# Performance work log

Measured on AMD Instinct MI355X. Metric: run time of the kernel, lower is better.

The kernel has to match this reference:

```python
import jax, jax.numpy as jnp
import numpy as np

N = 100000      # nodes
E = 800000      # edges (nnz of sparse adj)
D_IN = 128      # input feature dim
H = 64          # hidden_units
EMB = 32        # embsize
N_IDX = 50000   # gathered output rows
EPS = 1e-05     # BatchNormalization epsilon


def spmm(rows, cols, vals, x):
    # out[i] = sum_{e: rows[e]==i} vals[e] * x[cols[e]]  == sparse A @ x
    return jax.ops.segment_sum(vals[:, None] * x[cols], rows, num_segments=N)


def batchnorm(x, gamma, beta):
    # training-mode BN over node (batch) axis, matching Keras BatchNormalization
    m = jnp.mean(x, axis=0)
    v = jnp.var(x, axis=0)
    return (x - m) * jax.lax.rsqrt(v + EPS) * gamma + beta


def setup_inputs() -> dict:
    key = jax.random.key(0)
    ks = jax.random.split(key, 16)
    def w(k, fan_in, shape):
        return jax.random.normal(k, shape, dtype=jnp.float32) / np.sqrt(fan_in)
    inp = {
        "features": jax.random.normal(ks[0], (N, D_IN), dtype=jnp.float32),
        "rows": jax.random.randint(ks[1], (E,), 0, N),
        "cols": jax.random.randint(ks[2], (E,), 0, N),
        "vals": jax.random.uniform(ks[3], (E,), dtype=jnp.float32),
        "idx": jax.random.randint(ks[4], (N_IDX,), 0, N),
        # layer 0 (Dense with bias since l==0)
        "Wn0": w(ks[5], D_IN, (D_IN, H)), "bn0": jnp.zeros((H,), jnp.float32),
        "Wg0": w(ks[6], D_IN, (D_IN, H)), "bg0": jnp.zeros((H,), jnp.float32),
        "ab0": jnp.zeros((H,), jnp.float32),  # BiasLayer after SpMM
        "g0": jnp.ones((H,), jnp.float32), "b0": jnp.zeros((H,), jnp.float32),
        # layer 1 (no Dense bias)
        "Wn1": w(ks[7], H, (H, H)),
        "Wg1": w(ks[8], H, (H, H)),
        "ab1": jnp.zeros((H,), jnp.float32),
        "g1": jnp.ones((H,), jnp.float32), "b1": jnp.zeros((H,), jnp.float32),
        # conv_last block (Dense use_bias=False)
        "WnL": w(ks[9], H, (H, EMB)),
        "WgL": w(ks[10], H, (H, EMB)),
        "abL": jnp.zeros((EMB,), jnp.float32),
    }
    return inp


def reference(features, rows, cols, vals, idx,
              Wn0, bn0, Wg0, bg0, ab0, g0, b0,
              Wn1, Wg1, ab1, g1, b1,
              WnL, WgL, abL):
    x = features
    # SAGE layer 0
    x_node = x @ Wn0 + bn0
    x_neigh = x @ Wg0 + bg0
    agg = spmm(rows, cols, vals, x_neigh) + ab0
    x = jax.nn.relu(batchnorm(x_node + agg, g0, b0))
    # SAGE layer 1
    x_node = x @ Wn1
    x_neigh = x @ Wg1
    agg = spmm(rows, cols, vals, x_neigh) + ab1
    x = jax.nn.relu(batchnorm(x_node + agg, g1, b1))
    # conv_last projection to embsize
    x_node = x @ WnL
    x_neigh = x @ WgL
    agg = spmm(rows, cols, vals, x_neigh) + abL
    x = x_node + agg
    return x[idx]
```

## Files before the change

kernel.cpp:

```cpp
#include <hip/hip_runtime.h>

#define NNODES 100000
#define NEDGES 800000
#define DIN    128
#define HID    64
#define EMB    32
#define NIDX   50000
#define BN_EPS 1e-5f

#define NCHK 64
#define EC   (NEDGES / NCHK)
#define SUBC 256
#define ECS  (NEDGES / SUBC)
#define SPC  (SUBC / NCHK)
#define NB   ((NNODES + 63) / 64)
#define PF   16
#define NBF  ((NB + PF - 1) / PF)

typedef __attribute__((ext_vector_type(8))) short short8;
typedef __attribute__((ext_vector_type(4))) float f32x4;

__device__ inline unsigned short f2bf(float f) {
    unsigned u = __float_as_uint(f);
    unsigned r = u + 0x7FFFu + ((u >> 16) & 1u);
    return (unsigned short)(r >> 16);
}
__device__ inline float bf2f_lo(unsigned u) { return __uint_as_float(u << 16); }
__device__ inline float bf2f_hi(unsigned u) { return __uint_as_float(u & 0xffff0000u); }


__device__ inline void pack_seg(const float* __restrict__ Wn, const float* __restrict__ Wg,
                                unsigned short* __restrict__ Wp, int HOUT, int l2nt, int f) {
    int j = f & 7, lane = (f >> 3) & 63, g = f >> 9;
    int tt = g & ((1 << l2nt) - 1), kb = g >> l2nt;
    int k = kb * 32 + ((lane >> 4) * 8) + j;
    int nn = tt * 16 + (lane & 15);
    float v = (nn < HOUT) ? Wn[k * HOUT + nn] : Wg[k * HOUT + (nn - HOUT)];
    Wp[f] = f2bf(v);
}


__global__ __launch_bounds__(256) void histpack_k(
    const int* __restrict__ rows, int* __restrict__ Bcnt4,
    const int* __restrict__ idx, int* __restrict__ mark,
    const float* Wn0, const float* Wg0, const float* Wn1,
    const float* Wg1, const float* WnL, const float* WgL,
    unsigned short* Wp0, unsigned short* Wp1, unsigned short* WpL, int MB)
{
    int blk = blockIdx.x;
    if (blk >= SUBC + MB) {
        int f = (blk - SUBC - MB) * 256 + threadIdx.x;
        if (f < 16384)      pack_seg(Wn0, Wg0, Wp0, 64, 3, f);
        else if (f < 24576) pack_seg(Wn1, Wg1, Wp1, 64, 3, f - 16384);
        else if (f < 28672) pack_seg(WnL, WgL, WpL, 32, 2, f - 24576);
        return;
    }
    if (blk >= SUBC) {
        int j = (blk - SUBC) * 256 + threadIdx.x;
        if (j < NIDX) mark[idx[j]] = 1;
        return;
    }
    __shared__ int hist[NB];
    int t = threadIdx.x;
    for (int b = t; b < NB; b += 256) hist[b] = 0;
    __syncthreads();
    for (int i = t; i < ECS; i += 256)
        atomicAdd(&hist[rows[blk * ECS + i] >> 6], 1);
    __syncthreads();
    for (int b = t; b < NB; b += 256) Bcnt4[blk * NB + b] = hist[b];
}

__global__ void bprefix_k(const int* __restrict__ Bcnt4, int* __restrict__ BcntT,
                          int* __restrict__ bTot) {
    int b = blockIdx.x * 256 + threadIdx.x;
    if (b >= NB) return;
    int run = 0;
    for (int sub = 0; sub < SUBC; sub++) {
        if ((sub & (SPC - 1)) == 0)
            BcntT[(sub / SPC) * NB + b] = run;
        run += Bcnt4[sub * NB + b];
    }
    bTot[b] = run;
}

__global__ void bscan_k(const int* __restrict__ bTot, int* __restrict__ bBase) {
    __shared__ int s[256];
    int t = threadIdx.x;
    int v[7], loc = 0;
#pragma unroll
    for (int i = 0; i < 7; i++) {
        int ix = t * 7 + i;
        v[i] = loc;
        loc += (ix < NB) ? bTot[ix] : 0;
    }
    s[t] = loc;
    __syncthreads();
    for (int off = 1; off < 256; off <<= 1) {
        int a = (t >= off) ? s[t - off] : 0;
        __syncthreads();
        s[t] += a;
        __syncthreads();
    }
    int base = s[t] - loc;
#pragma unroll
    for (int i = 0; i < 7; i++) {
        int ix = t * 7 + i;
        if (ix < NB) bBase[ix] = base + v[i];
    }
    if (t == 255) bBase[NB] = NEDGES;
}

__global__ __launch_bounds__(256) void bfinal_k(const uint2* __restrict__ ebuf,
                                                const int* __restrict__ bBase,
                                                int* __restrict__ rowptr,
                                                int2* __restrict__ cs) {
    __shared__ int hist[64], sc[64], cur[64];
    int b = blockIdx.x, t = threadIdx.x;
    int e0 = bBase[b], e1 = bBase[b + 1];
    int r0 = b << 6;
    if (t < 64) hist[t] = 0;
    __syncthreads();
    for (int i = e0 + t; i < e1; i += 256)
        atomicAdd(&hist[(ebuf[i].x >> 20) & 63], 1);
    __syncthreads();
    if (t == 0) {
        int run = e0;
        for (int j = 0; j < 64; j++) { sc[j] = run; run += hist[j]; }
    }
    __syncthreads();
    if (t < 64) {
        cur[t] = sc[t];
        int r = r0 + t;
        if (r < NNODES) rowptr[r] = sc[t];
    }
    if (b == NB - 1 && t == 0) rowptr[NNODES] = NEDGES;
    __syncthreads();
    for (int i = e0 + t; i < e1; i += 256) {
        uint2 v = ebuf[i];
        int p = atomicAdd(&cur[(v.x >> 20) & 63], 1);
        cs[p] = make_int2((int)(v.x & 0xFFFFF), (int)v.y);
    }
}


template <int K, int HOUT, bool AFF, bool XBF, bool HNBF>
__device__ void gemm_body(const void* __restrict__ Xv, const unsigned short* __restrict__ Wp,
                          const float* __restrict__ bnA, const float* __restrict__ bnB,
                          const float* __restrict__ bgA,
                          const float* __restrict__ sums, const float* __restrict__ gamma,
                          const float* __restrict__ beta,
                          float* __restrict__ Hnf, unsigned short* __restrict__ Hnb,
                          unsigned short* __restrict__ Hgb, int n, int blk)
{
    constexpr int NT = 2 * HOUT / 16, NKB = K / 32;
    constexpr int RS = K + 8;
    constexpr int OC = HNBF ? 2 * HOUT : HOUT;
    constexpr int RSE = OC + 8;
    constexpr int XSZ = (RS > RSE) ? RS : RSE;
    __shared__ unsigned short Xs[64 * XSZ];
    __shared__ float sSc[64], sSh[64];

    const int row0 = blk * 64;
    const int t = threadIdx.x;

    if (AFF) {
        if (t < 64) {
            float sum = 0.f, sq = 0.f;
#pragma unroll
            for (int s = 0; s < 8; s++) { sum += sums[s * 128 + t]; sq += sums[s * 128 + 64 + t]; }
            float m = sum / (float)NNODES;
            float var = sq / (float)NNODES - m * m;
            float sc = gamma[t] * rsqrtf(var + BN_EPS);
            sSc[t] = sc; sSh[t] = beta[t] - m * sc;
        }
        __syncthreads();
    }

    constexpr int SIT = K / 32;
    if constexpr (XBF) {
        uint4 u[SIT];
#pragma unroll
        for (int it = 0; it < SIT; it++) {
            int li = it * 256 + t;
            int rr = row0 + li / (K / 8);
            int k8 = (li % (K / 8)) * 8;
            int rc = rr < n ? rr : n - 1;
            u[it] = *(const uint4*)((const unsigned short*)Xv + (size_t)rc * K + k8);
        }
#pragma unroll
        for (int it = 0; it < SIT; it++) {
            int li = it * 256 + t;
            int r  = li / (K / 8);
            int k8 = (li % (K / 8)) * 8;
            float v[8];
            v[0] = bf2f_lo(u[it].x); v[1] = bf2f_hi(u[it].x);
            v[2] = bf2f_lo(u[it].y); v[3] = bf2f_hi(u[it].y);
            v[4] = bf2f_lo(u[it].z); v[5] = bf2f_hi(u[it].z);
            v[6] = bf2f_lo(u[it].w); v[7] = bf2f_hi(u[it].w);
            if (AFF) {
#pragma unroll
                for (int i = 0; i < 8; i++) v[i] = fmaxf(v[i] * sSc[k8 + i] + sSh[k8 + i], 0.f);
            }
            uint4 o;
            o.x = (unsigned)f2bf(v[0]) | ((unsigned)f2bf(v[1]) << 16);
            o.y = (unsigned)f2bf(v[2]) | ((unsigned)f2bf(v[3]) << 16);
            o.z = (unsigned)f2bf(v[4]) | ((unsigned)f2bf(v[5]) << 16);
            o.w = (unsigned)f2bf(v[6]) | ((unsigned)f2bf(v[7]) << 16);
            *(uint4*)&Xs[r * RS + k8] = o;
        }
    } else {
        const float* Xf = (const float*)Xv;
        float4 a[SIT], b[SIT];
#pragma unroll
        for (int it = 0; it < SIT; it++) {
            int li = it * 256 + t;
            int rr = row0 + li / (K / 8);
            int k8 = (li % (K / 8)) * 8;
            int rc = rr < n ? rr : n - 1;
            a[it] = *(const float4*)&Xf[(size_t)rc * K + k8];
            b[it] = *(const float4*)&Xf[(size_t)rc * K + k8 + 4];
        }
#pragma unroll
        for (int it = 0; it < SIT; it++) {
            int li = it * 256 + t;
            int r  = li / (K / 8);
            int k8 = (li % (K / 8)) * 8;
            float v[8] = { a[it].x, a[it].y, a[it].z, a[it].w,
                           b[it].x, b[it].y, b[it].z, b[it].w };
            if (AFF) {
#pragma unroll
                for (int i = 0; i < 8; i++) v[i] = fmaxf(v[i] * sSc[k8 + i] + sSh[k8 + i], 0.f);
            }
            uint4 o;
            o.x = (unsigned)f2bf(v[0]) | ((unsigned)f2bf(v[1]) << 16);
            o.y = (unsigned)f2bf(v[2]) | ((unsigned)f2bf(v[3]) << 16);
            o.z = (unsigned)f2bf(v[4]) | ((unsigned)f2bf(v[5]) << 16);
            o.w = (unsigned)f2bf(v[6]) | ((unsigned)f2bf(v[7]) << 16);
            *(uint4*)&Xs[r * RS + k8] = o;
        }
    }
    __syncthreads();

    const int wave = t >> 6, lane = t & 63;
    const int q = lane >> 4, mrow = lane & 15;

    f32x4 acc[NT];
#pragma unroll
    for (int i = 0; i < NT; i++) acc[i] = (f32x4){0.f, 0.f, 0.f, 0.f};

    const short8* wp8 = (const short8*)Wp;
#pragma unroll
    for (int kb = 0; kb < NKB; kb++) {
        short8 va = *(const short8*)&Xs[(wave * 16 + mrow) * RS + kb * 32 + q * 8];
#pragma unroll
        for (int tt = 0; tt < NT; tt++) {
            short8 vb = wp8[(kb * NT + tt) * 64 + lane];
            acc[tt] = __builtin_amdgcn_mfma_f32_16x16x32_bf16(va, vb, acc[tt], 0, 0, 0);
        }
    }

    __syncthreads();
#pragma unroll
    for (int tt = 0; tt < NT; tt++) {
        int nglob = tt * 16 + mrow;
        bool nside = (nglob < HOUT);
        int c = nside ? nglob : (nglob - HOUT);
        float bias = 0.f;
        if (nside) {
            if (bnA) bias += bnA[c];
            if (bnB) bias += bnB[c];
        } else if (bgA) {
            bias += bgA[c];
        }
        if (HNBF || !nside) {
            int cc = HNBF ? nglob : c;
#pragma unroll
            for (int r = 0; r < 4; r++)
                Xs[(wave * 16 + q * 4 + r) * RSE + cc] = f2bf(acc[tt][r] + bias);
        } else {
#pragma unroll
            for (int r = 0; r < 4; r++) {
                int rr = row0 + wave * 16 + q * 4 + r;
                if (rr < n) Hnf[(size_t)rr * HOUT + c] = acc[tt][r] + bias;
            }
        }
    }
    __syncthreads();
    constexpr int J = OC / 8;
#pragma unroll
    for (int u2 = 0; u2 < (64 * J) / 256; u2++) {
        int li = u2 * 256 + t;
        int r = li / J, j = li % J;
        int rr = row0 + r;
        if (rr < n) {
            uint4 v = *(const uint4*)&Xs[r * RSE + j * 8];
            int c8 = j * 8;
            if (HNBF && c8 < HOUT)
                *(uint4*)&Hnb[(size_t)rr * HOUT + c8] = v;
            else
                *(uint4*)&Hgb[(size_t)rr * HOUT + (HNBF ? c8 - HOUT : c8)] = v;
        }
    }
}

__global__ __launch_bounds__(256) void part_gemm0_k(
    const int* __restrict__ rows, const int* __restrict__ cols,
    const float* __restrict__ vals, const int* __restrict__ BcntT,
    const int* __restrict__ bBase, uint2* __restrict__ ebuf,
    const float* __restrict__ X, const unsigned short* __restrict__ Wp0,
    const float* __restrict__ bn0, const float* __restrict__ ab0, const float* __restrict__ bg0,
    unsigned short* __restrict__ Hn0b, unsigned short* __restrict__ Hgb, int n)
{
    if ((int)blockIdx.x < NCHK * PF) {
        __shared__ int cur[NBF];
        int t = threadIdx.x;
        int blk = blockIdx.x % NCHK;
        int pf  = blockIdx.x / NCHK;
        int b0 = pf * NBF, b1 = (pf == PF - 1) ? NB : (b0 + NBF);
        for (int b = b0 + t; b < b1; b += 256)
            cur[b - b0] = bBase[b] + BcntT[blk * NB + b];
        __syncthreads();
        constexpr int EC4 = EC / 4;
        const int*   rbase = rows + blk * EC;
        const int*   cbase = cols + blk * EC;
        const float* vbase = vals + blk * EC;
        for (int i4 = t; i4 < EC4; i4 += 256) {
            int4   r4 = *(const int4*)&rbase[i4 * 4];
            int4   c4 = *(const int4*)&cbase[i4 * 4];
            float4 v4 = *(const float4*)&vbase[i4 * 4];
#pragma unroll
            for (int j = 0; j < 4; j++) {
                int r = (&r4.x)[j];
                int b = r >> 6;
                if (b >= b0 && b < b1) {
                    int p = atomicAdd(&cur[b - b0], 1);
                    ebuf[p] = make_uint2(((unsigned)(r & 63) << 20) | (unsigned)(&c4.x)[j],
                                         (unsigned)__float_as_int((&v4.x)[j]));
                }
            }
        }
    } else {
        gemm_body<DIN, HID, false, false, true>(X, Wp0, bn0, ab0, bg0,
            nullptr, nullptr, nullptr, nullptr, Hn0b, Hgb, n, blockIdx.x - NCHK * PF);
    }
}

template <int K, int HOUT, bool AFF, bool XBF, bool HNBF>
__global__ __launch_bounds__(256) void gemm_k(
    const void* __restrict__ X, const unsigned short* __restrict__ Wp,
    const float* __restrict__ bnA, const float* __restrict__ bnB, const float* __restrict__ bgA,
    const float* __restrict__ sums, const float* __restrict__ gamma, const float* __restrict__ beta,
    float* __restrict__ Hnf, unsigned short* __restrict__ Hnb, unsigned short* __restrict__ Hgb, int n)
{
    gemm_body<K, HOUT, AFF, XBF, HNBF>(X, Wp, bnA, bnB, bgA, sums, gamma, beta,
                                       Hnf, Hnb, Hgb, n, blockIdx.x);
}


template <int HH, bool STATS, bool SBF, bool MARKED>
__global__ __launch_bounds__(256) void spmm_k(
    const int* __restrict__ rowptr, const int2* __restrict__ cs,
    const unsigned short* __restrict__ Hgb, void* __restrict__ Sv,
    float* __restrict__ stats, const int* __restrict__ mark, int n)
{
    constexpr int L   = HH / 4;
    constexpr int GP  = 256 / L;
    constexpr int RPB = 64;
    constexpr int RPG = RPB / GP;
    constexpr int ECAP = 1024;
    __shared__ int2 es[ECAP];
    __shared__ int  rp[RPB + 1];

    const int t = threadIdx.x;
    const int R0 = blockIdx.x * RPB;
    if (t <= RPB) rp[t] = rowptr[min(R0 + t, n)];
    __syncthreads();
    const int e0b  = rp[0];
    const int scnt = min(rp[RPB] - e0b, ECAP);
    for (int i = t; i < scnt; i += 256) es[i] = cs[e0b + i];
    __syncthreads();

    const int lane = t % L;
    const int g    = t / L;
    const int c0   = lane * 4;

    float4 sum = make_float4(0.f, 0.f, 0.f, 0.f);
    float4 sq  = make_float4(0.f, 0.f, 0.f, 0.f);

#define SPMM_ROW(FETCH)                                                            \
    {                                                                              \
        int e = le0;                                                               \
        for (; e + 3 < le1; e += 4) {                                              \
            int2 p0 = FETCH(e), p1 = FETCH(e + 1), p2 = FETCH(e + 2), p3 = FETCH(e + 3); \
            float v0 = __int_as_float(p0.y), v1 = __int_as_float(p1.y);            \
            float v2 = __int_as_float(p2.y), v3 = __int_as_float(p3.y);            \
            uint2 h0 = *(const uint2*)&Hgb[(size_t)p0.x * HH + c0];                \
            uint2 h1 = *(const uint2*)&Hgb[(size_t)p1.x * HH + c0];                \
            uint2 h2 = *(const uint2*)&Hgb[(size_t)p2.x * HH + c0];                \
            uint2 h3 = *(const uint2*)&Hgb[(size_t)p3.x * HH + c0];                \
            a0.x += v0 * bf2f_lo(h0.x); a0.y += v0 * bf2f_hi(h0.x);                \
            a0.z += v0 * bf2f_lo(h0.y); a0.w += v0 * bf2f_hi(h0.y);                \
            a1.x += v1 * bf2f_lo(h1.x); a1.y += v1 * bf2f_hi(h1.x);                \
            a1.z += v1 * bf2f_lo(h1.y); a1.w += v1 * bf2f_hi(h1.y);                \
            a2.x += v2 * bf2f_lo(h2.x); a2.y += v2 * bf2f_hi(h2.x);                \
            a2.z += v2 * bf2f_lo(h2.y); a2.w += v2 * bf2f_hi(h2.y);                \
            a3.x += v3 * bf2f_lo(h3.x); a3.y += v3 * bf2f_hi(h3.x);                \
            a3.z += v3 * bf2f_lo(h3.y); a3.w += v3 * bf2f_hi(h3.y);                \
        }                                                                          \
        for (; e < le1; e++) {                                                     \
            int2 p = FETCH(e);                                                     \
            float v = __int_as_float(p.y);                                         \
            uint2 h = *(const uint2*)&Hgb[(size_t)p.x * HH + c0];                  \
            a0.x += v * bf2f_lo(h.x); a0.y += v * bf2f_hi(h.x);                    \
            a0.z += v * bf2f_lo(h.y); a0.w += v * bf2f_hi(h.y);                    \
        }                                                                          \
    }
#define F_LDS(i) es[(i)]
#define F_GLB(i) cs[e0b + (i)]

#pragma unroll
    for (int rr = 0; rr < RPG; rr++) {
        int row = R0 + g * RPG + rr;
        if (row >= n) break;
        if (MARKED && !mark[row]) continue;
        int le0 = rp[g * RPG + rr] - e0b;
        int le1 = rp[g * RPG + rr + 1] - e0b;
        float4 a0, a1, a2, a3;
        if (SBF) {
            uint2 h = *(const uint2*)((const unsigned short*)Sv + (size_t)row * HH + c0);
            a0 = make_float4(bf2f_lo(h.x), bf2f_hi(h.x), bf2f_lo(h.y), bf2f_hi(h.y));
        } else {
            a0 = *(const float4*)((const float*)Sv + (size_t)row * HH + c0);
        }
        a1 = a2 = a3 = make_float4(0.f, 0.f, 0.f, 0.f);
        if (le1 <= scnt) SPMM_ROW(F_LDS) else SPMM_ROW(F_GLB);
        float4 acc = make_float4(a0.x + a1.x + a2.x + a3.x, a0.y + a1.y + a2.y + a3.y,
                                 a0.z + a1.z + a2.z + a3.z, a0.w + a1.w + a2.w + a3.w);
        if (SBF) {
            uint2 o;
            o.x = (unsigned)f2bf(acc.x) | ((unsigned)f2bf(acc.y) << 16);
            o.y = (unsigned)f2bf(acc.z) | ((unsigned)f2bf(acc.w) << 16);
            *(uint2*)((unsigned short*)Sv + (size_t)row * HH + c0) = o;
        } else {
            *(float4*)((float*)Sv + (size_t)row * HH + c0) = acc;
        }
        if (STATS) {
            sum.x += acc.x; sum.y += acc.y; sum.z += acc.z; sum.w += acc.w;
            sq.x += acc.x * acc.x; sq.y += acc.y * acc.y;
            sq.z += acc.z * acc.z; sq.w += acc.w * acc.w;
        }
    }
#undef SPMM_ROW
#undef F_LDS
#undef F_GLB

    if constexpr (STATS) {
        __shared__ float rs[GP][HH];
        __shared__ float rq[GP][HH];
        *(float4*)&rs[g][c0] = sum;
        *(float4*)&rq[g][c0] = sq;
        __syncthreads();
        if (threadIdx.x < HH) {
            float a = 0.f, b = 0.f;
            for (int w = 0; w < GP; w++) { a += rs[w][threadIdx.x]; b += rq[w][threadIdx.x]; }
            int stripe = blockIdx.x & 7;
            atomicAdd(&stats[stripe * 128 + threadIdx.x], a);
            atomicAdd(&stats[stripe * 128 + HH + threadIdx.x], b);
        }
    }
}

__global__ void gather_k(const float* __restrict__ S, const int* __restrict__ idx,
                         float* __restrict__ out, int total4) {
    int j = blockIdx.x * 256 + threadIdx.x;
    if (j < total4) {
        int r = j / (EMB / 4), c4 = (j % (EMB / 4)) * 4;
        *(float4*)&out[(size_t)j * 4] = *(const float4*)&S[(size_t)idx[r] * EMB + c4];
    }
}


extern "C" void kernel_launch(void* const* d_in, const int* in_sizes, int n_in,
                              void* d_out, int out_size, void* d_ws, size_t ws_size,
                              hipStream_t stream) {
    const float* features = (const float*)d_in[0];
    const int*   rows     = (const int*)d_in[1];
    const int*   cols     = (const int*)d_in[2];
    const float* vals     = (const float*)d_in[3];
    const int*   idx      = (const int*)d_in[4];
    const float* Wn0 = (const float*)d_in[5];
    const float* bn0 = (const float*)d_in[6];
    const float* Wg0 = (const float*)d_in[7];
    const float* bg0 = (const float*)d_in[8];
    const float* ab0 = (const float*)d_in[9];
    const float* g0  = (const float*)d_in[10];
    const float* b0  = (const float*)d_in[11];
    const float* Wn1 = (const float*)d_in[12];
    const float* Wg1 = (const float*)d_in[13];
    const float* ab1 = (const float*)d_in[14];
    const float* g1  = (const float*)d_in[15];
    const float* b1  = (const float*)d_in[16];
    const float* WnL = (const float*)d_in[17];
    const float* WgL = (const float*)d_in[18];
    const float* abL = (const float*)d_in[19];
    float* out = (float*)d_out;

    float*          HnLf = (float*)d_ws;
    unsigned short* nA   = (unsigned short*)(HnLf + (size_t)NNODES * EMB);
    unsigned short* nB   = nA + (size_t)NNODES * HID;
    unsigned short* Hgb  = nB + (size_t)NNODES * HID;
    uint2* ebuf  = (uint2*)(Hgb + (size_t)NNODES * HID);
    int2*  cs    = (int2*)(ebuf + NEDGES);
    int*   rowptr = (int*)(cs + NEDGES);
    int*   Bcnt4 = rowptr + (NNODES + 4);
    int*   BcntT = Bcnt4 + SUBC * NB;
    int*   bTot  = BcntT + NCHK * NB;
    int*   bBase = bTot + 1568;
    unsigned short* Wp0 = (unsigned short*)(bBase + 1568);
    unsigned short* Wp1 = Wp0 + 16384;
    unsigned short* WpL = Wp1 + 8192;
    float* stats = (float*)(WpL + 4096);
    int*   mark  = (int*)(stats + 2304);
    float* sums0 = stats;
    float* sums1 = stats + 1024;
    size_t zbytes = 2304 * 4 + (size_t)NNODES * 4;

    hipMemsetAsync(stats, 0, zbytes, stream);

    const int GBm = (NNODES + 63) / 64;
    const int MB  = (NIDX + 255) / 256;

    histpack_k<<<SUBC + MB + 112, 256, 0, stream>>>(
        rows, Bcnt4, idx, mark, Wn0, Wg0, Wn1, Wg1, WnL, WgL, Wp0, Wp1, WpL, MB);
    bprefix_k<<<7, 256, 0, stream>>>(Bcnt4, BcntT, bTot);
    bscan_k<<<1, 256, 0, stream>>>(bTot, bBase);
    part_gemm0_k<<<NCHK * PF + GBm, 256, 0, stream>>>(rows, cols, vals, BcntT, bBase, ebuf,
                                                      features, Wp0, bn0, ab0, bg0,
                                                      nA, Hgb, NNODES);
    bfinal_k<<<NB, 256, 0, stream>>>(ebuf, bBase, rowptr, cs);

    spmm_k<HID, true, true, false><<<GBm, 256, 0, stream>>>(rowptr, cs, Hgb, nA, sums0, nullptr, NNODES);

    gemm_k<HID, HID, true, true, true><<<GBm, 256, 0, stream>>>(
        nA, Wp1, ab1, nullptr, nullptr, sums0, g0, b0, nullptr, nB, Hgb, NNODES);
    spmm_k<HID, true, true, false><<<GBm, 256, 0, stream>>>(rowptr, cs, Hgb, nB, sums1, nullptr, NNODES);

    gemm_k<HID, EMB, true, true, false><<<GBm, 256, 0, stream>>>(
        nB, WpL, abL, nullptr, nullptr, sums1, g1, b1, HnLf, nullptr, Hgb, NNODES);
    spmm_k<EMB, false, false, true><<<GBm, 256, 0, stream>>>(rowptr, cs, Hgb, HnLf, nullptr, mark, NNODES);

    gather_k<<<(NIDX * EMB / 4 + 255) / 256, 256, 0, stream>>>(HnLf, idx, out, NIDX * EMB / 4);
}
```

Before: 278.0 us.

## Fuse CSR bucket finalization with the first SpMM layer

Merges the kernel that builds rowptr/col-value pairs for each 64-row bucket with the layer-0 SpMM and BN statistics accumulation. Each block reuses its just-written CSR segment (from shared histogram offsets) to aggregate neighbor features, add the node term, write bf16 output and atomically add column sums and squares. This removes one kernel launch and a re-read of rowptr, at the cost of reading cs right after writing it within the same block and using fewer threads per row (16 lanes × 4 rows per group).

```diff
diff --git a/kernel.cpp b/kernel.cpp
--- a/kernel.cpp
+++ b/kernel.cpp
@@ -110,11 +110,15 @@
     if (t == 255) bBase[NB] = NEDGES;
 }
 
-__global__ __launch_bounds__(256) void bfinal_k(const uint2* __restrict__ ebuf,
-                                                const int* __restrict__ bBase,
-                                                int* __restrict__ rowptr,
-                                                int2* __restrict__ cs) {
+
+__global__ __launch_bounds__(256) void bfinal_spmm0_k(
+    const uint2* __restrict__ ebuf, const int* __restrict__ bBase,
+    int* __restrict__ rowptr, int2* __restrict__ cs,
+    const unsigned short* __restrict__ Hgb, unsigned short* __restrict__ S,
+    float* __restrict__ stats, int n)
+{
     __shared__ int hist[64], sc[64], cur[64];
+    __shared__ float rs[16][HID], rq[16][HID];
     int b = blockIdx.x, t = threadIdx.x;
     int e0 = bBase[b], e1 = bBase[b + 1];
     int r0 = b << 6;
@@ -139,6 +143,67 @@
         uint2 v = ebuf[i];
         int p = atomicAdd(&cur[(v.x >> 20) & 63], 1);
         cs[p] = make_int2((int)(v.x & 0xFFFFF), (int)v.y);
+    }
+    __syncthreads();
+
+    const int lane = t & 15, g = t >> 4;
+    const int c0 = lane * 4;
+    float4 sum = make_float4(0.f, 0.f, 0.f, 0.f);
+    float4 sq  = make_float4(0.f, 0.f, 0.f, 0.f);
+#pragma unroll
+    for (int rr = 0; rr < 4; rr++) {
+        int lr = g * 4 + rr;
+        int row = r0 + lr;
+        if (row >= n) break;
+        int le0 = sc[lr], le1 = sc[lr] + hist[lr];
+        uint2 h = *(const uint2*)&S[(size_t)row * HID + c0];
+        float4 a0 = make_float4(bf2f_lo(h.x), bf2f_hi(h.x), bf2f_lo(h.y), bf2f_hi(h.y));
+        float4 a1 = make_float4(0.f, 0.f, 0.f, 0.f), a2 = a1, a3 = a1;
+        int e = le0;
+        for (; e + 3 < le1; e += 4) {
+            int2 p0 = cs[e], p1 = cs[e + 1], p2 = cs[e + 2], p3 = cs[e + 3];
+            float v0 = __int_as_float(p0.y), v1 = __int_as_float(p1.y);
+            float v2 = __int_as_float(p2.y), v3 = __int_as_float(p3.y);
+            uint2 h0 = *(const uint2*)&Hgb[(size_t)p0.x * HID + c0];
+            uint2 h1 = *(const uint2*)&Hgb[(size_t)p1.x * HID + c0];
+            uint2 h2 = *(const uint2*)&Hgb[(size_t)p2.x * HID + c0];
+            uint2 h3 = *(const uint2*)&Hgb[(size_t)p3.x * HID + c0];
+            a0.x += v0 * bf2f_lo(h0.x); a0.y += v0 * bf2f_hi(h0.x);
+            a0.z += v0 * bf2f_lo(h0.y); a0.w += v0 * bf2f_hi(h0.y);
+            a1.x += v1 * bf2f_lo(h1.x); a1.y += v1 * bf2f_hi(h1.x);
+            a1.z += v1 * bf2f_lo(h1.y); a1.w += v1 * bf2f_hi(h1.y);
+            a2.x += v2 * bf2f_lo(h2.x); a2.y += v2 * bf2f_hi(h2.x);
+            a2.z += v2 * bf2f_lo(h2.y); a2.w += v2 * bf2f_hi(h2.y);
+            a3.x += v3 * bf2f_lo(h3.x); a3.y += v3 * bf2f_hi(h3.x);
+            a3.z += v3 * bf2f_lo(h3.y); a3.w += v3 * bf2f_hi(h3.y);
+        }
+        for (; e < le1; e++) {
+            int2 p = cs[e];
+            float v = __int_as_float(p.y);
+            uint2 hh = *(const uint2*)&Hgb[(size_t)p.x * HID + c0];
+            a0.x += v * bf2f_lo(hh.x); a0.y += v * bf2f_hi(hh.x);
+            a0.z += v * bf2f_lo(hh.y); a0.w += v * bf2f_hi(hh.y);
+        }
+        float4 acc = make_float4(a0.x + a1.x + a2.x + a3.x, a0.y + a1.y + a2.y + a3.y,
+                                 a0.z + a1.z + a2.z + a3.z, a0.w + a1.w + a2.w + a3.w);
+        uint2 o;
+        o.x = (unsigned)f2bf(acc.x) | ((unsigned)f2bf(acc.y) << 16);
+        o.y = (unsigned)f2bf(acc.z) | ((unsigned)f2bf(acc.w) << 16);
+        *(uint2*)&S[(size_t)row * HID + c0] = o;
+        sum.x += acc.x; sum.y += acc.y; sum.z += acc.z; sum.w += acc.w;
+        sq.x += acc.x * acc.x; sq.y += acc.y * acc.y;
+        sq.z += acc.z * acc.z; sq.w += acc.w * acc.w;
+    }
+
+    *(float4*)&rs[g][c0] = sum;
+    *(float4*)&rq[g][c0] = sq;
+    __syncthreads();
+    if (t < HID) {
+        float a = 0.f, bb = 0.f;
+        for (int w = 0; w < 16; w++) { a += rs[w][t]; bb += rq[w][t]; }
+        int stripe = b & 7;
+        atomicAdd(&stats[stripe * 128 + t], a);
+        atomicAdd(&stats[stripe * 128 + HID + t], bb);
     }
 }
 
@@ -537,9 +602,7 @@
     part_gemm0_k<<<NCHK * PF + GBm, 256, 0, stream>>>(rows, cols, vals, BcntT, bBase, ebuf,
                                                       features, Wp0, bn0, ab0, bg0,
                                                       nA, Hgb, NNODES);
-    bfinal_k<<<NB, 256, 0, stream>>>(ebuf, bBase, rowptr, cs);
-
-    spmm_k<HID, true, true, false><<<GBm, 256, 0, stream>>>(rowptr, cs, Hgb, nA, sums0, nullptr, NNODES);
+    bfinal_spmm0_k<<<NB, 256, 0, stream>>>(ebuf, bBase, rowptr, cs, Hgb, nA, sums0, NNODES);
 
     gemm_k<HID, HID, true, true, true><<<GBm, 256, 0, stream>>>(
         nA, Wp1, ab1, nullptr, nullptr, sums0, g0, b0, nullptr, nB, Hgb, NNODES);
```

Measured after the change: 276.0 us. No clear change (-0.7%).
